# Kernel optimization log

Measured on AMD Instinct MI355X. Metric: run time of the kernel, lower is better.

Reference implementation:

```python
import jax, jax.numpy as jnp
import numpy as np

N, V, NJ, NB, NP = 512, 6890, 24, 10, 207
PARENTS = np.array([0, 0, 0, 0, 1, 2, 3, 4, 5, 6, 7, 8, 9, 9, 9, 12, 13, 14, 16, 17, 18, 19, 20, 21], dtype=np.int32)


def setup_inputs() -> dict:
    key = jax.random.key(0)
    ks = jax.random.split(key, 10)
    # near-rotation matrices (math does not require orthonormality since theta_is_perfect_rotmtx=True)
    pose = jnp.eye(3, dtype=jnp.float32) + 0.1 * jax.random.normal(ks[0], (N, NJ, 3, 3), dtype=jnp.float32)
    betas = jax.random.normal(ks[1], (N, NB), dtype=jnp.float32)
    trans = jax.random.normal(ks[2], (N, 3), dtype=jnp.float32)
    v_template = 0.02 * jax.random.normal(ks[3], (V, 3), dtype=jnp.float32)
    # ensure body_height (used for 1.66/height scaling) is well away from zero
    v_template = v_template.at[jnp.array([2802, 6262]), 1].add(1.0)
    shapedirs = 0.01 * jax.random.normal(ks[4], (NB, V * 3), dtype=jnp.float32)
    J_regressor = jax.random.uniform(ks[5], (NJ, V), dtype=jnp.float32) / V
    posedirs = 0.01 * jax.random.normal(ks[6], (NP, V * 3), dtype=jnp.float32)
    lbs_weights = jax.nn.softmax(jax.random.normal(ks[7], (V, NJ), dtype=jnp.float32), axis=-1)
    body25_reg = jax.random.uniform(ks[8], (25, V), dtype=jnp.float32) / V
    face_reg = jax.random.uniform(ks[9], (70, V), dtype=jnp.float32) / V
    return {
        "pose": pose, "betas": betas, "trans": trans,
        "v_template": v_template, "shapedirs": shapedirs,
        "J_regressor": J_regressor, "posedirs": posedirs,
        "lbs_weights": lbs_weights, "body25_reg": body25_reg,
        "face_reg": face_reg, "parents": jnp.asarray(PARENTS),
    }


def _fk(Rs, Js, parents):
    """batch_global_rigid_transformation: Rs [N,24,3,3], Js [N,24,3] -> (new_J [N,24,3], A [N,24,4,4])."""
    n = Rs.shape[0]
    Js_e = Js[..., None]                       # N,24,3,1
    ones = jnp.ones((n, 1, 1), Rs.dtype)

    def make_A(R, t):                          # R [N,3,3], t [N,3,1] -> [N,4,4]
        R_h = jnp.pad(R, ((0, 0), (0, 1), (0, 0)))
        t_h = jnp.concatenate([t, ones], axis=1)
        return jnp.concatenate([R_h, t_h], axis=2)

    results = [make_A(Rs[:, 0], Js_e[:, 0])]
    for i in range(1, NJ):                     # strictly sequential parent chain (fixed 24 joints)
        p = int(parents[i])
        j_here = Js_e[:, i] - Js_e[:, p]
        results.append(results[p] @ make_A(Rs[:, i], j_here))
    res = jnp.stack(results, axis=1)           # N,24,4,4
    new_J = res[:, :, :3, 3]
    Js_w0 = jnp.concatenate([Js_e, jnp.zeros((n, NJ, 1, 1), Rs.dtype)], axis=2)  # N,24,4,1
    init_bone = jnp.pad(res @ Js_w0, ((0, 0), (0, 0), (0, 0), (3, 0)))           # N,24,4,4
    return new_J, res - init_bone


def reference(pose, betas, trans, v_template, shapedirs, J_regressor, posedirs,
              lbs_weights, body25_reg, face_reg, parents):
    parents = np.asarray(parents)
    n = betas.shape[0]
    # shape blendshapes
    v_ss = (betas @ shapedirs).reshape(n, V, 3) + v_template            # v_shaped_scaled
    body_height = v_ss[:, 2802, 1] + v_ss[:, 6262, 1] - (v_ss[:, 2237, 1] + v_ss[:, 6728, 1])
    scale = (1.66 / body_height)[:, None, None]
    v_shaped = scale * v_ss                                             # v_personal = 0
    J = scale * jnp.einsum('jv,nvc->njc', J_regressor, v_ss)
    # pose blendshapes
    Rs = pose                                                           # theta_is_perfect_rotmtx
    pose_feature = (Rs[:, 1:] - jnp.eye(3, dtype=Rs.dtype)).reshape(n, NP)
    v_posed = (pose_feature @ posedirs).reshape(n, V, 3) + v_shaped
    # forward kinematics + LBS
    _, A = _fk(Rs, J, parents)
    T = jnp.einsum('vj,njab->nvab', lbs_weights, A)                     # N,V,4,4
    v_h = jnp.concatenate([v_posed, jnp.ones((n, V, 1), v_posed.dtype)], axis=2)
    verts = jnp.einsum('nvab,nvb->nva', T, v_h)[:, :, :3] + trans[:, None]
    j25 = jnp.einsum('kv,nvc->nkc', body25_reg, verts)
    fl = jnp.einsum('kv,nvc->nkc', face_reg, verts)
    return jnp.concatenate([j25, fl], axis=1)                           # N,95,3
```

## Files before the change

kernel.cpp:

```cpp
#include <hip/hip_runtime.h>


constexpr int N   = 512;
constexpr int V   = 6890;
constexpr int V3  = V * 3;
constexpr int NJ  = 24;
constexpr int NB  = 10;
constexpr int NP  = 207;
constexpr int NK  = 95;
constexpr int KP  = 224;
constexpr int VP2 = 6912;

constexpr size_t SCALE_OFF = (size_t)N * V3;
constexpr size_t SJ_OFF    = SCALE_OFF + N;
constexpr size_t JT_OFF    = SJ_OFF + (size_t)NB * 72;
constexpr size_t J_OFF     = JT_OFF + 72;
constexpr size_t A_OFF     = J_OFF + (size_t)N * 72;
constexpr size_t BF_OFF    = A_OFF + (size_t)N * 288;
constexpr size_t APF_U     = 0;
constexpr int    BP_COLS   = 20736;
constexpr size_t BP_U      = (size_t)N * KP;
constexpr size_t RB_U      = BP_U + (size_t)BP_COLS * KP;
constexpr size_t VB_U      = RB_U + (size_t)96 * VP2;
constexpr size_t BF_END_U  = VB_U + (size_t)N * 3 * VP2;
constexpr size_t WT_OFF    = BF_OFF + (BF_END_U + 1) / 2;
constexpr size_t AN_OFF    = WT_OFF + (size_t)VP2 * 32 / 2;

constexpr int NB_REGBF = (96 * VP2) / 256;
constexpr int NB_BT    = BP_COLS / 64;
constexpr int NB_WT    = VP2 / 256;
constexpr int NB_PRE   = 72;
constexpr int NB_STATIC = NB_REGBF + NB_BT + NB_WT + NB_PRE;

typedef short s16x8 __attribute__((ext_vector_type(8)));
typedef _Float16 h16x8 __attribute__((ext_vector_type(8)));
typedef _Float16 h16x4 __attribute__((ext_vector_type(4)));
typedef float f32x4 __attribute__((ext_vector_type(4)));

__device__ inline unsigned short f2bf(float f) {
    unsigned u = __float_as_uint(f);
    u += 0x7fffu + ((u >> 16) & 1u);
    return (unsigned short)(u >> 16);
}

__global__ __launch_bounds__(256) void k_static(const float* __restrict__ pdirs,
                                                const float* __restrict__ sd,
                                                const float* __restrict__ jreg,
                                                const float* __restrict__ vt,
                                                const float* __restrict__ lbsw,
                                                const float* __restrict__ b25,
                                                const float* __restrict__ face,
                                                unsigned short* __restrict__ bp,
                                                _Float16* __restrict__ rb,
                                                _Float16* __restrict__ w16,
                                                float* __restrict__ ws) {
    __shared__ unsigned short smem[KP * 66];
    int b = blockIdx.x;
    int tid = threadIdx.x;

    if (b < NB_REGBF) {
        int t = b * 256 + tid;
        int k = t / VP2, v = t - k * VP2;
        float val = 0.f;
        if (v < V && k < NK)
            val = (k < 25) ? b25[(size_t)k * V + v] : face[(size_t)(k - 25) * V + v];
        int kt = k >> 4, m16 = k & 15;
        int step = v >> 5, q8 = (v >> 3) & 3, j = v & 7;
        rb[((size_t)(kt * 216 + step) * 64 + q8 * 16 + m16) * 8 + j] = (_Float16)val;
        return;
    }
    b -= NB_REGBF;
    if (b < NB_BT) {
        int c0 = b * 64;
#pragma unroll 4
        for (int i = 0; i < 56; ++i) {
            int e = tid + 256 * i;
            int k = e >> 6, cl = e & 63;
            int col = c0 + cl;
            float v = 0.f;
            if (col < V3) {
                if (k < NP) v = pdirs[(size_t)k * V3 + col];
                else if (k < NP + NB) v = sd[(size_t)(k - NP) * V3 + col];
            }
            smem[k * 66 + cl] = f2bf(v);
        }
        __syncthreads();
        for (int i = 0; i < 7; ++i) {
            int u = tid + 256 * i;
            int ct_loc = u / 448;
            int rem = u - ct_loc * 448;
            int kk = rem >> 6, lane = rem & 63;
            int m = lane & 15, q = lane >> 4;
            s16x8 r;
#pragma unroll
            for (int j = 0; j < 8; ++j)
                r[j] = (short)smem[(kk * 32 + q * 8 + j) * 66 + ct_loc * 16 + m];
            size_t ctg = (size_t)(c0 >> 4) + ct_loc;
            *reinterpret_cast<s16x8*>(&bp[((ctg * 7 + kk) * 64 + lane) * 8]) = r;
        }
        return;
    }
    b -= NB_BT;
    if (b < NB_WT) {
        float* t = reinterpret_cast<float*>(smem);
        int v0 = b * 256;
        for (int e = tid; e < 256 * 24; e += 256) {
            int g = v0 * 24 + e;
            float val = (g < V * NJ) ? lbsw[g] : 0.f;
            int vv = e / 24, j = e - vv * 24;
            t[vv * 25 + j] = val;
        }
        __syncthreads();
        _Float16* dst = w16 + (size_t)(v0 + tid) * 32;
#pragma unroll
        for (int j = 0; j < 32; ++j)
            dst[j] = (j < NJ) ? (_Float16)t[tid * 25 + j] : (_Float16)0.f;
        return;
    }
    b -= NB_WT;
    int jc = b;
    int j = jc / 3, c = jc % 3;
    float acc[NB + 1];
#pragma unroll
    for (int t = 0; t <= NB; ++t) acc[t] = 0.f;
    for (int v = tid; v < V; v += 256) {
        float w = jreg[(size_t)j * V + v];
        int col = v * 3 + c;
#pragma unroll
        for (int k = 0; k < NB; ++k) acc[k] += w * sd[(size_t)k * V3 + col];
        acc[NB] += w * vt[col];
    }
    float* red = reinterpret_cast<float*>(smem);
    int lane = tid & 63, w64 = tid >> 6;
#pragma unroll
    for (int t = 0; t <= NB; ++t) {
        float a = acc[t];
#pragma unroll
        for (int s = 1; s < 64; s <<= 1) a += __shfl_xor(a, s, 64);
        if (lane == 0) red[w64 * 16 + t] = a;
    }
    __syncthreads();
    if (tid <= NB) {
        float s = red[tid] + red[16 + tid] + red[32 + tid] + red[48 + tid];
        if (tid < NB) ws[SJ_OFF + (size_t)tid * 72 + jc] = s;
        else          ws[JT_OFF + jc] = s;
    }
}

__global__ __launch_bounds__(64) void k_head(const float* __restrict__ pose,
                                             const float* __restrict__ betas,
                                             const float* __restrict__ vt,
                                             const float* __restrict__ sd,
                                             float* __restrict__ ws,
                                             unsigned short* __restrict__ apf,
                                             _Float16* __restrict__ an16) {
    int n = blockIdx.x;
    int tid = threadIdx.x;
    __shared__ float sval[4];
    __shared__ float Jl[NJ * 3];
    __shared__ float G[NJ * 12];
    __shared__ unsigned short pfsh[KP];

    const int idx4[4] = {2802 * 3 + 1, 6262 * 3 + 1, 2237 * 3 + 1, 6728 * 3 + 1};
    if (tid < 4) {
        float a = vt[idx4[tid]];
#pragma unroll
        for (int k = 0; k < NB; ++k)
            a += betas[n * NB + k] * sd[(size_t)k * V3 + idx4[tid]];
        sval[tid] = a;
    }
    __syncthreads();
    float scale = 1.66f / (sval[0] + sval[1] - sval[2] - sval[3]);
    if (tid == 0) ws[SCALE_OFF + n] = scale;

    for (int k = tid; k < KP; k += 64) {
        float v = 0.f;
        if (k < NP) {
            v = pose[(size_t)n * 216 + 9 + k];
            int km = k % 9;
            if (km == 0 || km == 4 || km == 8) v -= 1.f;
        } else if (k < NP + NB) {
            v = scale * betas[n * NB + (k - NP)];
        }
        pfsh[k] = f2bf(v);
    }
    for (int e = tid; e < 72; e += 64) {
        float a = ws[JT_OFF + e];
#pragma unroll
        for (int k = 0; k < NB; ++k)
            a += betas[n * NB + k] * ws[SJ_OFF + (size_t)k * 72 + e];
        Jl[e] = scale * a;
    }
    __syncthreads();
    if (tid < 28) {
        int kk = tid >> 2, q = tid & 3;
        s16x8 r;
#pragma unroll
        for (int j = 0; j < 8; ++j) r[j] = (short)pfsh[kk * 32 + q * 8 + j];
        size_t off = ((size_t)(n >> 4) * 7 + kk) * 64 + q * 16 + (n & 15);
        *reinterpret_cast<s16x8*>(&apf[off * 8]) = r;
    }

    const int par[NJ] = {0,0,0,0,1,2,3,4,5,6,7,8,9,9,9,12,13,14,16,17,18,19,20,21};
    if (tid < 12) {
        int r = tid >> 2, c = tid & 3;
        G[tid] = (c < 3) ? pose[(size_t)n * 216 + r * 3 + c] : Jl[r];
    }
    __syncthreads();
    for (int i = 1; i < NJ; ++i) {
        int p = par[i];
        if (tid < 12) {
            int r = tid >> 2, c = tid & 3;
            const float* gp = &G[p * 12 + r * 4];
            float v;
            if (c < 3) {
                const float* Ri = pose + (size_t)n * 216 + i * 9;
                v = gp[0] * Ri[0 * 3 + c] + gp[1] * Ri[1 * 3 + c] + gp[2] * Ri[2 * 3 + c];
            } else {
                float t0 = Jl[i * 3 + 0] - Jl[p * 3 + 0];
                float t1 = Jl[i * 3 + 1] - Jl[p * 3 + 1];
                float t2 = Jl[i * 3 + 2] - Jl[p * 3 + 2];
                v = gp[0] * t0 + gp[1] * t1 + gp[2] * t2 + gp[3];
            }
            G[i * 12 + tid] = v;
        }
        __syncthreads();
    }
    for (int e = tid; e < 512; e += 64) {
        int col = e >> 5, j = e & 31;
        float v = 0.f;
        if (col < 12 && j < NJ) {
            int r = col >> 2, c = col & 3;
            if (c < 3) v = G[j * 12 + r * 4 + c];
            else {
                const float* g = &G[j * 12 + r * 4];
                v = g[3] - (g[0] * Jl[j * 3 + 0] + g[1] * Jl[j * 3 + 1] + g[2] * Jl[j * 3 + 2]);
            }
        }
        an16[(size_t)n * 512 + e] = (_Float16)v;
    }
}

__global__ __launch_bounds__(256) void k_gl(const unsigned short* __restrict__ apf,
                                            const unsigned short* __restrict__ bp,
                                            const float* __restrict__ vt,
                                            const float* __restrict__ ws,
                                            const _Float16* __restrict__ w16,
                                            const _Float16* __restrict__ an16,
                                            const float* __restrict__ trans,
                                            _Float16* __restrict__ vb) {
    int tid = threadIdx.x;
    int lane = tid & 63, w = tid >> 6;
    int m = lane & 15, q = lane >> 4;
    int cb = blockIdx.x;
    int nb = blockIdx.y;
    int wg = w & 1;
    int wc = w >> 1;

    __shared__ __align__(16) _Float16 sm[32][33][4];
    __shared__ float svt[96];
    __shared__ float ssc[32];
    __shared__ float strans[96];
    if (tid < 96) {
        int col = cb * 96 + tid;
        svt[tid] = (col < V3) ? vt[col] : 0.f;
        strans[tid] = trans[nb * 96 + tid];
    }
    if (tid < 32) ssc[tid] = ws[SCALE_OFF + nb * 32 + tid];

    const unsigned short* abase = apf + (size_t)(nb * 2 + wg) * 7 * 512 + lane * 8;
    const unsigned short* bbase = bp + (size_t)(cb * 6 + wc * 3) * 7 * 512 + lane * 8;

    f32x4 acc[3];
#pragma unroll
    for (int ct = 0; ct < 3; ++ct) acc[ct] = (f32x4){0.f, 0.f, 0.f, 0.f};

#pragma unroll
    for (int kk = 0; kk < 7; ++kk) {
        s16x8 a = *reinterpret_cast<const s16x8*>(abase + kk * 512);
#pragma unroll
        for (int ct = 0; ct < 3; ++ct) {
            s16x8 bfr = *reinterpret_cast<const s16x8*>(bbase + (ct * 7 + kk) * 512);
            acc[ct] = __builtin_amdgcn_mfma_f32_16x16x32_bf16(a, bfr, acc[ct], 0, 0, 0);
        }
    }

    h16x8 wf[2];
#pragma unroll
    for (int g = 0; g < 2; ++g)
        wf[g] = *reinterpret_cast<const h16x8*>(
            &w16[(size_t)(cb * 32 + g * 16 + m) * 32 + q * 8]);

    __syncthreads();
#pragma unroll
    for (int ct = 0; ct < 3; ++ct) {
        int col_loc = (wc * 3 + ct) * 16 + m;
        int v_loc = col_loc / 3;
        int c = col_loc - 3 * v_loc;
        float vtc = svt[col_loc];
#pragma unroll
        for (int r = 0; r < 4; ++r) {
            int n_loc = wg * 16 + q * 4 + r;
            sm[n_loc][v_loc][c] = (_Float16)(acc[ct][r] + ssc[n_loc] * vtc);
        }
    }

    __syncthreads();

    const _Float16* anb = an16 + (size_t)(nb * 32 + w * 8) * 512 + m * 32 + q * 8;
    _Float16* vbase = vb + (size_t)(nb * 32 + w * 8) * 3 * VP2 + (size_t)q * VP2
                      + (size_t)cb * 32;
#pragma unroll
    for (int half = 0; half < 2; ++half) {
        h16x8 bf8[4];
#pragma unroll
        for (int i = 0; i < 4; ++i)
            bf8[i] = *reinterpret_cast<const h16x8*>(anb + (size_t)(half * 4 + i) * 512);
#pragma unroll
        for (int i = 0; i < 4; ++i) {
            int nl = w * 8 + half * 4 + i;
            f32x4 at[2];
#pragma unroll
            for (int g = 0; g < 2; ++g) {
                f32x4 z = (f32x4){0.f, 0.f, 0.f, 0.f};
                at[g] = __builtin_amdgcn_mfma_f32_16x16x32_f16(bf8[i], wf[g], z, 0, 0, 0);
            }
            if (q < 3) {
                float tr = strans[nl * 3 + q];
#pragma unroll
                for (int g = 0; g < 2; ++g) {
                    int vl = g * 16 + m;
                    h16x4 p = *reinterpret_cast<const h16x4*>(&sm[nl][vl][0]);
                    float r = at[g][0] * (float)p[0] + at[g][1] * (float)p[1]
                            + at[g][2] * (float)p[2] + at[g][3] + tr;
                    vbase[(size_t)(half * 4 + i) * 3 * VP2 + vl] = (_Float16)r;
                }
            }
        }
    }
}

__global__ __launch_bounds__(256) void k_regm(const _Float16* __restrict__ rb,
                                              const _Float16* __restrict__ vb,
                                              float* __restrict__ out) {
    int tid = threadIdx.x;
    int lane = tid & 63, w = tid >> 6;
    int m = lane & 15, q = lane >> 4;
    int nct = blockIdx.x;
    int split = blockIdx.y;

    const _Float16* brow = vb + (size_t)(nct * 16 + m) * VP2 + q * 8;
    const _Float16* abase = rb + (size_t)(q * 16 + m) * 8;
    int vstart = (split * 4 + w) * 288;
    int stepBase = (split * 4 + w) * 9;

    f32x4 acc[6];
#pragma unroll
    for (int kt = 0; kt < 6; ++kt) acc[kt] = (f32x4){0.f, 0.f, 0.f, 0.f};

#pragma unroll
    for (int s = 0; s < 9; ++s) {
        int off = vstart + s * 32;
        h16x8 b = *reinterpret_cast<const h16x8*>(brow + off);
#pragma unroll
        for (int kt = 0; kt < 6; ++kt) {
            h16x8 a = *reinterpret_cast<const h16x8*>(
                abase + ((size_t)(kt * 216 + stepBase + s) << 9));
            acc[kt] = __builtin_amdgcn_mfma_f32_16x16x32_f16(a, b, acc[kt], 0, 0, 0);
        }
    }
    __shared__ float sm[4][6][256];
#pragma unroll
    for (int kt = 0; kt < 6; ++kt)
#pragma unroll
        for (int r = 0; r < 4; ++r)
            sm[w][kt][(q * 4 + r) * 16 + m] = acc[kt][r];
    __syncthreads();
    for (int e = tid; e < 6 * 256; e += 256) {
        int kt = e >> 8, i = e & 255;
        float s = sm[0][kt][i] + sm[1][kt][i] + sm[2][kt][i] + sm[3][kt][i];
        int k = kt * 16 + (i >> 4);
        int nc = nct * 16 + (i & 15);
        if (k < NK) {
            int n = nc / 3, c = nc - n * 3;
            atomicAdd(&out[(size_t)n * (NK * 3) + k * 3 + c], s);
        }
    }
}

extern "C" void kernel_launch(void* const* d_in, const int* in_sizes, int n_in,
                              void* d_out, int out_size, void* d_ws, size_t ws_size,
                              hipStream_t stream) {
    const float* pose  = (const float*)d_in[0];
    const float* betas = (const float*)d_in[1];
    const float* trans = (const float*)d_in[2];
    const float* vt    = (const float*)d_in[3];
    const float* sd    = (const float*)d_in[4];
    const float* jreg  = (const float*)d_in[5];
    const float* pdirs = (const float*)d_in[6];
    const float* lbsw  = (const float*)d_in[7];
    const float* b25   = (const float*)d_in[8];
    const float* face  = (const float*)d_in[9];
    float* ws  = (float*)d_ws;
    float* out = (float*)d_out;
    unsigned short* bf  = (unsigned short*)(ws + BF_OFF);
    unsigned short* apf = bf + APF_U;
    unsigned short* bp  = bf + BP_U;
    _Float16* rb  = (_Float16*)(bf + RB_U);
    _Float16* vb  = (_Float16*)(bf + VB_U);
    _Float16* w16 = (_Float16*)(ws + WT_OFF);
    _Float16* an16 = (_Float16*)(ws + AN_OFF);

    hipMemsetAsync(d_out, 0, (size_t)out_size * sizeof(float), stream);

    k_static<<<NB_STATIC, 256, 0, stream>>>(pdirs, sd, jreg, vt, lbsw, b25, face,
                                            bp, rb, w16, ws);
    k_head  <<<N, 64, 0, stream>>>(pose, betas, vt, sd, ws, apf, an16);
    k_gl    <<<dim3(216, 16), 256, 0, stream>>>(apf, bp, vt, ws, w16, an16, trans, vb);
    k_regm  <<<dim3(96, 6), 256, 0, stream>>>(rb, vb, out);
}
```

Baseline: 163.9 us.

## Merge per-sample head work into static prep kernel and rebalance regression split

New measurement: 170.8 us. 4.2% more time.

```diff
diff --git a/kernel.cpp b/kernel.cpp
--- a/kernel.cpp
+++ b/kernel.cpp
@@ -26,11 +26,11 @@
 constexpr size_t WT_OFF    = BF_OFF + (BF_END_U + 1) / 2;
 constexpr size_t AN_OFF    = WT_OFF + (size_t)VP2 * 32 / 2;
 
-constexpr int NB_REGBF = (96 * VP2) / 256;
+constexpr int NB_HEAD  = N / 4;
+constexpr int NB_REGBF = (96 * VP2) / (256 * 8);
 constexpr int NB_BT    = BP_COLS / 64;
 constexpr int NB_WT    = VP2 / 256;
-constexpr int NB_PRE   = 72;
-constexpr int NB_STATIC = NB_REGBF + NB_BT + NB_WT + NB_PRE;
+constexpr int NB_PREP  = NB_HEAD + NB_REGBF + NB_BT + NB_WT;
 
 typedef short s16x8 __attribute__((ext_vector_type(8)));
 typedef _Float16 h16x8 __attribute__((ext_vector_type(8)));
@@ -43,34 +43,171 @@
     return (unsigned short)(u >> 16);
 }
 
-__global__ __launch_bounds__(256) void k_static(const float* __restrict__ pdirs,
-                                                const float* __restrict__ sd,
-                                                const float* __restrict__ jreg,
-                                                const float* __restrict__ vt,
-                                                const float* __restrict__ lbsw,
-                                                const float* __restrict__ b25,
-                                                const float* __restrict__ face,
-                                                unsigned short* __restrict__ bp,
-                                                _Float16* __restrict__ rb,
-                                                _Float16* __restrict__ w16,
-                                                float* __restrict__ ws) {
-    __shared__ unsigned short smem[KP * 66];
+__global__ __launch_bounds__(256) void k_pre(const float* __restrict__ jreg,
+                                             const float* __restrict__ sd,
+                                             const float* __restrict__ vt,
+                                             float* __restrict__ ws) {
+    int jc = blockIdx.x;
+    int tid = threadIdx.x;
+    int j = jc / 3, c = jc % 3;
+    float acc[NB + 1];
+#pragma unroll
+    for (int t = 0; t <= NB; ++t) acc[t] = 0.f;
+    for (int v = tid; v < V; v += 256) {
+        float w = jreg[(size_t)j * V + v];
+        int col = v * 3 + c;
+#pragma unroll
+        for (int k = 0; k < NB; ++k) acc[k] += w * sd[(size_t)k * V3 + col];
+        acc[NB] += w * vt[col];
+    }
+    __shared__ float red[64];
+    int lane = tid & 63, w64 = tid >> 6;
+#pragma unroll
+    for (int t = 0; t <= NB; ++t) {
+        float a = acc[t];
+#pragma unroll
+        for (int s = 1; s < 64; s <<= 1) a += __shfl_xor(a, s, 64);
+        if (lane == 0) red[w64 * 16 + t] = a;
+    }
+    __syncthreads();
+    if (tid <= NB) {
+        float s = red[tid] + red[16 + tid] + red[32 + tid] + red[48 + tid];
+        if (tid < NB) ws[SJ_OFF + (size_t)tid * 72 + jc] = s;
+        else          ws[JT_OFF + jc] = s;
+    }
+}
+
+__global__ __launch_bounds__(256) void k_prep(const float* __restrict__ pdirs,
+                                              const float* __restrict__ sd,
+                                              const float* __restrict__ vt,
+                                              const float* __restrict__ lbsw,
+                                              const float* __restrict__ b25,
+                                              const float* __restrict__ face,
+                                              const float* __restrict__ pose,
+                                              const float* __restrict__ betas,
+                                              unsigned short* __restrict__ bp,
+                                              _Float16* __restrict__ rb,
+                                              _Float16* __restrict__ w16,
+                                              unsigned short* __restrict__ apf,
+                                              _Float16* __restrict__ an16,
+                                              float* __restrict__ ws) {
+    __shared__ __align__(16) unsigned char smbuf[KP * 66 * 2];
     int b = blockIdx.x;
     int tid = threadIdx.x;
 
+    if (b < NB_HEAD) {
+        int w = tid >> 6, ln = tid & 63;
+        int n = b * 4 + w;
+        float* fbase = reinterpret_cast<float*>(smbuf);
+        float* sval = fbase + w * 4;
+        float* Jl   = fbase + 16 + w * 72;
+        float* G    = fbase + 304 + w * 288;
+        unsigned short* pfsh =
+            reinterpret_cast<unsigned short*>(fbase + 1456) + w * KP;
+
+        const int idx4[4] = {2802 * 3 + 1, 6262 * 3 + 1, 2237 * 3 + 1, 6728 * 3 + 1};
+        if (ln < 4) {
+            float a = vt[idx4[ln]];
+#pragma unroll
+            for (int k = 0; k < NB; ++k)
+                a += betas[n * NB + k] * sd[(size_t)k * V3 + idx4[ln]];
+            sval[ln] = a;
+        }
+        __syncthreads();
+        float scale = 1.66f / (sval[0] + sval[1] - sval[2] - sval[3]);
+        if (ln == 0) ws[SCALE_OFF + n] = scale;
+
+        for (int k = ln; k < KP; k += 64) {
+            float v = 0.f;
+            if (k < NP) {
+                v = pose[(size_t)n * 216 + 9 + k];
+                int km = k % 9;
+                if (km == 0 || km == 4 || km == 8) v -= 1.f;
+            } else if (k < NP + NB) {
+                v = scale * betas[n * NB + (k - NP)];
+            }
+            pfsh[k] = f2bf(v);
+        }
+        for (int e = ln; e < 72; e += 64) {
+            float a = ws[JT_OFF + e];
+#pragma unroll
+            for (int k = 0; k < NB; ++k)
+                a += betas[n * NB + k] * ws[SJ_OFF + (size_t)k * 72 + e];
+            Jl[e] = scale * a;
+        }
+        __syncthreads();
+        if (ln < 28) {
+            int kk = ln >> 2, q = ln & 3;
+            s16x8 r;
+#pragma unroll
+            for (int j = 0; j < 8; ++j) r[j] = (short)pfsh[kk * 32 + q * 8 + j];
+            size_t off = ((size_t)(n >> 4) * 7 + kk) * 64 + q * 16 + (n & 15);
+            *reinterpret_cast<s16x8*>(&apf[off * 8]) = r;
+        }
+
+        const int par[NJ] = {0,0,0,0,1,2,3,4,5,6,7,8,9,9,9,12,13,14,16,17,18,19,20,21};
+        if (ln < 12) {
+            int r = ln >> 2, c = ln & 3;
+            G[ln] = (c < 3) ? pose[(size_t)n * 216 + r * 3 + c] : Jl[r];
+        }
+        __syncthreads();
+        for (int i = 1; i < NJ; ++i) {
+            int p = par[i];
+            if (ln < 12) {
+                int r = ln >> 2, c = ln & 3;
+                const float* gp = &G[p * 12 + r * 4];
+                float v;
+                if (c < 3) {
+                    const float* Ri = pose + (size_t)n * 216 + i * 9;
+                    v = gp[0] * Ri[0 * 3 + c] + gp[1] * Ri[1 * 3 + c] + gp[2] * Ri[2 * 3 + c];
+                } else {
+                    float t0 = Jl[i * 3 + 0] - Jl[p * 3 + 0];
+                    float t1 = Jl[i * 3 + 1] - Jl[p * 3 + 1];
+                    float t2 = Jl[i * 3 + 2] - Jl[p * 3 + 2];
+                    v = gp[0] * t0 + gp[1] * t1 + gp[2] * t2 + gp[3];
+                }
+                G[i * 12 + ln] = v;
+            }
+            __syncthreads();
+        }
+        for (int e = ln; e < 512; e += 64) {
+            int col = e >> 5, j = e & 31;
+            float v = 0.f;
+            if (col < 12 && j < NJ) {
+                int r = col >> 2, c = col & 3;
+                if (c < 3) v = G[j * 12 + r * 4 + c];
+                else {
+                    const float* g = &G[j * 12 + r * 4];
+                    v = g[3] - (g[0] * Jl[j * 3 + 0] + g[1] * Jl[j * 3 + 1]
+                              + g[2] * Jl[j * 3 + 2]);
+                }
+            }
+            an16[(size_t)n * 512 + e] = (_Float16)v;
+        }
+        return;
+    }
+    b -= NB_HEAD;
     if (b < NB_REGBF) {
-        int t = b * 256 + tid;
-        int k = t / VP2, v = t - k * VP2;
-        float val = 0.f;
-        if (v < V && k < NK)
-            val = (k < 25) ? b25[(size_t)k * V + v] : face[(size_t)(k - 25) * V + v];
+        int t0 = (b * 256 + tid) * 8;
+        int k = t0 / VP2, v = t0 - k * VP2;
+        h16x8 val;
+#pragma unroll
+        for (int j = 0; j < 8; ++j) {
+            float x = 0.f;
+            int vv = v + j;
+            if (vv < V && k < NK)
+                x = (k < 25) ? b25[(size_t)k * V + vv] : face[(size_t)(k - 25) * V + vv];
+            val[j] = (_Float16)x;
+        }
         int kt = k >> 4, m16 = k & 15;
-        int step = v >> 5, q8 = (v >> 3) & 3, j = v & 7;
-        rb[((size_t)(kt * 216 + step) * 64 + q8 * 16 + m16) * 8 + j] = (_Float16)val;
+        int step = v >> 5, q8 = (v >> 3) & 3;
+        *reinterpret_cast<h16x8*>(
+            &rb[((size_t)(kt * 216 + step) * 64 + q8 * 16 + m16) * 8]) = val;
         return;
     }
     b -= NB_REGBF;
     if (b < NB_BT) {
+        unsigned short* smem = reinterpret_cast<unsigned short*>(smbuf);
         int c0 = b * 64;
 #pragma unroll 4
         for (int i = 0; i < 56; ++i) {
@@ -101,8 +238,8 @@
         return;
     }
     b -= NB_BT;
-    if (b < NB_WT) {
-        float* t = reinterpret_cast<float*>(smem);
+    {
+        float* t = reinterpret_cast<float*>(smbuf);
         int v0 = b * 256;
         for (int e = tid; e < 256 * 24; e += 256) {
             int g = v0 * 24 + e;
@@ -115,129 +252,6 @@
 #pragma unroll
         for (int j = 0; j < 32; ++j)
             dst[j] = (j < NJ) ? (_Float16)t[tid * 25 + j] : (_Float16)0.f;
-        return;
-    }
-    b -= NB_WT;
-    int jc = b;
-    int j = jc / 3, c = jc % 3;
-    float acc[NB + 1];
-#pragma unroll
-    for (int t = 0; t <= NB; ++t) acc[t] = 0.f;
-    for (int v = tid; v < V; v += 256) {
-        float w = jreg[(size_t)j * V + v];
-        int col = v * 3 + c;
-#pragma unroll
-        for (int k = 0; k < NB; ++k) acc[k] += w * sd[(size_t)k * V3 + col];
-        acc[NB] += w * vt[col];
-    }
-    float* red = reinterpret_cast<float*>(smem);
-    int lane = tid & 63, w64 = tid >> 6;
-#pragma unroll
-    for (int t = 0; t <= NB; ++t) {
-        float a = acc[t];
-#pragma unroll
-        for (int s = 1; s < 64; s <<= 1) a += __shfl_xor(a, s, 64);
-        if (lane == 0) red[w64 * 16 + t] = a;
-    }
-    __syncthreads();
-    if (tid <= NB) {
-        float s = red[tid] + red[16 + tid] + red[32 + tid] + red[48 + tid];
-        if (tid < NB) ws[SJ_OFF + (size_t)tid * 72 + jc] = s;
-        else          ws[JT_OFF + jc] = s;
-    }
-}
-
-__global__ __launch_bounds__(64) void k_head(const float* __restrict__ pose,
-                                             const float* __restrict__ betas,
-                                             const float* __restrict__ vt,
-                                             const float* __restrict__ sd,
-                                             float* __restrict__ ws,
-                                             unsigned short* __restrict__ apf,
-                                             _Float16* __restrict__ an16) {
-    int n = blockIdx.x;
-    int tid = threadIdx.x;
-    __shared__ float sval[4];
-    __shared__ float Jl[NJ * 3];
-    __shared__ float G[NJ * 12];
-    __shared__ unsigned short pfsh[KP];
-
-    const int idx4[4] = {2802 * 3 + 1, 6262 * 3 + 1, 2237 * 3 + 1, 6728 * 3 + 1};
-    if (tid < 4) {
-        float a = vt[idx4[tid]];
-#pragma unroll
-        for (int k = 0; k < NB; ++k)
-            a += betas[n * NB + k] * sd[(size_t)k * V3 + idx4[tid]];
-        sval[tid] = a;
-    }
-    __syncthreads();
-    float scale = 1.66f / (sval[0] + sval[1] - sval[2] - sval[3]);
-    if (tid == 0) ws[SCALE_OFF + n] = scale;
-
-    for (int k = tid; k < KP; k += 64) {
-        float v = 0.f;
-        if (k < NP) {
-            v = pose[(size_t)n * 216 + 9 + k];
-            int km = k % 9;
-            if (km == 0 || km == 4 || km == 8) v -= 1.f;
-        } else if (k < NP + NB) {
-            v = scale * betas[n * NB + (k - NP)];
-        }
-        pfsh[k] = f2bf(v);
-    }
-    for (int e = tid; e < 72; e += 64) {
-        float a = ws[JT_OFF + e];
-#pragma unroll
-        for (int k = 0; k < NB; ++k)
-            a += betas[n * NB + k] * ws[SJ_OFF + (size_t)k * 72 + e];
-        Jl[e] = scale * a;
-    }
-    __syncthreads();
-    if (tid < 28) {
-        int kk = tid >> 2, q = tid & 3;
-        s16x8 r;
-#pragma unroll
-        for (int j = 0; j < 8; ++j) r[j] = (short)pfsh[kk * 32 + q * 8 + j];
-        size_t off = ((size_t)(n >> 4) * 7 + kk) * 64 + q * 16 + (n & 15);
-        *reinterpret_cast<s16x8*>(&apf[off * 8]) = r;
-    }
-
-    const int par[NJ] = {0,0,0,0,1,2,3,4,5,6,7,8,9,9,9,12,13,14,16,17,18,19,20,21};
-    if (tid < 12) {
-        int r = tid >> 2, c = tid & 3;
-        G[tid] = (c < 3) ? pose[(size_t)n * 216 + r * 3 + c] : Jl[r];
-    }
-    __syncthreads();
-    for (int i = 1; i < NJ; ++i) {
-        int p = par[i];
-        if (tid < 12) {
-            int r = tid >> 2, c = tid & 3;
-            const float* gp = &G[p * 12 + r * 4];
-            float v;
-            if (c < 3) {
-                const float* Ri = pose + (size_t)n * 216 + i * 9;
-                v = gp[0] * Ri[0 * 3 + c] + gp[1] * Ri[1 * 3 + c] + gp[2] * Ri[2 * 3 + c];
-            } else {
-                float t0 = Jl[i * 3 + 0] - Jl[p * 3 + 0];
-                float t1 = Jl[i * 3 + 1] - Jl[p * 3 + 1];
-                float t2 = Jl[i * 3 + 2] - Jl[p * 3 + 2];
-                v = gp[0] * t0 + gp[1] * t1 + gp[2] * t2 + gp[3];
-            }
-            G[i * 12 + tid] = v;
-        }
-        __syncthreads();
-    }
-    for (int e = tid; e < 512; e += 64) {
-        int col = e >> 5, j = e & 31;
-        float v = 0.f;
-        if (col < 12 && j < NJ) {
-            int r = col >> 2, c = col & 3;
-            if (c < 3) v = G[j * 12 + r * 4 + c];
-            else {
-                const float* g = &G[j * 12 + r * 4];
-                v = g[3] - (g[0] * Jl[j * 3 + 0] + g[1] * Jl[j * 3 + 1] + g[2] * Jl[j * 3 + 2]);
-            }
-        }
-        an16[(size_t)n * 512 + e] = (_Float16)v;
     }
 }
 
@@ -351,15 +365,16 @@
 
     const _Float16* brow = vb + (size_t)(nct * 16 + m) * VP2 + q * 8;
     const _Float16* abase = rb + (size_t)(q * 16 + m) * 8;
-    int vstart = (split * 4 + w) * 288;
-    int stepBase = (split * 4 + w) * 9;
+    int slot = split * 4 + w;
+    int vstart = slot * 192;
+    int stepBase = slot * 6;
 
     f32x4 acc[6];
 #pragma unroll
     for (int kt = 0; kt < 6; ++kt) acc[kt] = (f32x4){0.f, 0.f, 0.f, 0.f};
 
 #pragma unroll
-    for (int s = 0; s < 9; ++s) {
+    for (int s = 0; s < 6; ++s) {
         int off = vstart + s * 32;
         h16x8 b = *reinterpret_cast<const h16x8*>(brow + off);
 #pragma unroll
@@ -413,9 +428,9 @@
 
     hipMemsetAsync(d_out, 0, (size_t)out_size * sizeof(float), stream);
 
-    k_static<<<NB_STATIC, 256, 0, stream>>>(pdirs, sd, jreg, vt, lbsw, b25, face,
-                                            bp, rb, w16, ws);
-    k_head  <<<N, 64, 0, stream>>>(pose, betas, vt, sd, ws, apf, an16);
-    k_gl    <<<dim3(216, 16), 256, 0, stream>>>(apf, bp, vt, ws, w16, an16, trans, vb);
-    k_regm  <<<dim3(96, 6), 256, 0, stream>>>(rb, vb, out);
-}
+    k_pre <<<72, 256, 0, stream>>>(jreg, sd, vt, ws);
+    k_prep<<<NB_PREP, 256, 0, stream>>>(pdirs, sd, vt, lbsw, b25, face, pose, betas,
+                                        bp, rb, w16, apf, an16, ws);
+    k_gl  <<<dim3(216, 16), 256, 0, stream>>>(apf, bp, vt, ws, w16, an16, trans, vb);
+    k_regm<<<dim3(96, 9), 256, 0, stream>>>(rb, vb, out);
+}
```
